# Optimization experiments

Hardware: AMD Instinct MI355X
Metric: run time of the kernel (lower is better)

The kernel has to match this reference:

```python
import jax, jax.numpy as jnp
import numpy as np

B, L, K, I, O = 4, 10000, 16, 256, 256


def setup_inputs() -> dict:
    key = jax.random.key(0)
    k1, k2, k3 = jax.random.split(key, 3)
    x = jax.random.normal(k1, (B, L, I), dtype=jnp.float32)
    index_tensor = jax.random.randint(k2, (L, K), 0, L, dtype=jnp.int64)
    stdv = 0.5
    mask = jax.random.uniform(k3, (K, I, O), dtype=jnp.float32, minval=-stdv, maxval=stdv)
    bias = jnp.zeros((O,), dtype=jnp.float32)
    return {"x": x, "index_tensor": index_tensor, "mask": mask, "bias": bias}


def reference(x, index_tensor, mask, bias):
    # torch: expand x to [b,l,l,i], gather along dim2 with index[l,k] -> [b,l,k,i]
    # equivalent: per output node n, neighbors x[:, index_tensor[n, j], :]
    gathered = x[:, index_tensor, :]            # [b, l, k, i]
    # flatten(k,i) @ flatten(mask: [k*i, o]) == einsum over k,i
    y = jnp.einsum('blki,kio->blo', gathered, mask) + bias
    return y
```

## Files before the change

### kernel.cpp

```cpp
#include <hip/hip_runtime.h>

#define Bdim 4
#define Ldim 10000
#define Kdim 16
#define Idim 256
#define Odim 256

typedef __attribute__((ext_vector_type(8))) __bf16 bf16x8;
typedef __attribute__((ext_vector_type(4))) float f32x4;

__global__ __launch_bounds__(256)
void prepack(const float* __restrict__ x, const float* __restrict__ mask,
             __bf16* __restrict__ xb, __bf16* __restrict__ wpk)
{
    const int b = blockIdx.x;
    if (b < 2500) {
        const size_t base = ((size_t)b * 256 + threadIdx.x) * 16;
#pragma unroll
        for (int j = 0; j < 2; ++j) {
            const float4 f0 = *(const float4*)(x + base + j * 8);
            const float4 f1 = *(const float4*)(x + base + j * 8 + 4);
            bf16x8 v;
            v[0] = (__bf16)f0.x; v[1] = (__bf16)f0.y; v[2] = (__bf16)f0.z; v[3] = (__bf16)f0.w;
            v[4] = (__bf16)f1.x; v[5] = (__bf16)f1.y; v[6] = (__bf16)f1.z; v[7] = (__bf16)f1.w;
            *(bf16x8*)(xb + base + j * 8) = v;
        }
    } else {
        const int tg = (b - 2500) * 256 + threadIdx.x;
        const int c  = tg >> 6;
        const int ln = tg & 63;
        const int ni  = c & 3;
        const int ks  = (c >> 2) & 1;
        const int wid = (c >> 3) & 3;
        const int kb  = c >> 5;
        const int n   = wid * 64 + ni * 16 + (ln & 15);
        const int kk0 = kb * 64 + ks * 32 + (ln >> 4) * 8;
        bf16x8 v;
#pragma unroll
        for (int j = 0; j < 8; ++j)
            v[j] = (__bf16)mask[(size_t)(kk0 + j) * Odim + n];
        *(bf16x8*)(wpk + (size_t)tg * 8) = v;
    }
}

#define TL 8
#define BM 32
#define LDA 72

#define BARRIER() do { asm volatile("s_waitcnt lgkmcnt(0)" ::: "memory"); \
                       __builtin_amdgcn_s_barrier(); } while (0)

__global__ __launch_bounds__(256, 4)
void piconv_gemm(const __bf16* __restrict__ xb,
                 const int* __restrict__ idxT,
                 const __bf16* __restrict__ wpk,
                 const float* __restrict__ bias,
                 float* __restrict__ out)
{
    __shared__ __bf16 Alds[2][BM * LDA];
    __shared__ int    idx_lds[TL * Kdim];

    const int t    = threadIdx.x;
    const int l0   = blockIdx.x * TL;
    const int lane = t & 63;
    const int wid  = t >> 6;
    const int q    = lane >> 4;
    const int r16  = lane & 15;

    if (t < TL * Kdim)
        idx_lds[t] = idxT[l0 * Kdim + t];

    const int arow = t >> 3;
    const int apart = t & 7;
    const int alt  = arow & 7;
    const int abb  = arow >> 3;
    const size_t abase = ((size_t)abb * Ldim) << 8;

    const __bf16* wbase = wpk + ((size_t)(wid * 8) << 9) + lane * 8;

    f32x4  acc[2][4] = {};
    bf16x8 a0, a1;
    bf16x8 wA[8], wB[8];

    __syncthreads();

    {
        const int iv = idx_lds[alt * Kdim];
        const __bf16* s0 = xb + abase + (((size_t)iv) << 8) + apart * 8;
        a0 = *(const bf16x8*)s0;
#pragma unroll
        for (int j = 0; j < 8; ++j)
            wA[j] = *(const bf16x8*)(wbase + j * 512);
        a1 = *(const bf16x8*)(s0 + 64);
    }

#define STEP(S, BUF, AV, WCUR, WNXT, PFA, PFW)                                  \
    {                                                                           \
        *(bf16x8*)&Alds[BUF][arow * LDA + apart * 8] = AV;                      \
        BARRIER();                                                              \
        if (PFA) {                        \
            const int kn = ((S) + 2) >> 2;                                      \
            const int io = ((((S) + 2) & 3) << 6) + apart * 8;                  \
            const int iv = idx_lds[alt * Kdim + kn];                            \
            AV = *(const bf16x8*)(xb + abase + (((size_t)iv) << 8) + io);       \
        }                                                                       \
        if (PFW) {                                                  \
            const __bf16* wq = wbase + ((size_t)((S) + 1)) * 16384;             \
            _Pragma("unroll")                                                   \
            for (int j = 0; j < 8; ++j)                                         \
                WNXT[j] = *(const bf16x8*)(wq + j * 512);                       \
        }                                                                       \
        _Pragma("unroll")                                                       \
        for (int ks = 0; ks < 2; ++ks) {                                        \
            bf16x8 af[2];                                                       \
            _Pragma("unroll")                                                   \
            for (int mi = 0; mi < 2; ++mi)                                      \
                af[mi] = *(bf16x8*)&Alds[BUF][(mi * 16 + r16) * LDA + ks * 32 + q * 8]; \
            _Pragma("unroll")                                                   \
            for (int mi = 0; mi < 2; ++mi)                                      \
                _Pragma("unroll")                                               \
                for (int ni = 0; ni < 4; ++ni)                                  \
                    acc[mi][ni] = __builtin_amdgcn_mfma_f32_16x16x32_bf16(      \
                        af[mi], WCUR[ks * 4 + ni], acc[mi][ni], 0, 0, 0);       \
        }                                                                       \
    }

    for (int s2 = 0; s2 < 31; ++s2) {
        STEP(2 * s2,     0, a0, wA, wB, true, true)
        STEP(2 * s2 + 1, 1, a1, wB, wA, true, true)
    }
    STEP(62, 0, a0, wA, wB, false, true)
    STEP(63, 1, a1, wB, wA, false, false)
#undef STEP

    float bv[4];
#pragma unroll
    for (int ni = 0; ni < 4; ++ni)
        bv[ni] = bias[wid * 64 + ni * 16 + r16];
#pragma unroll
    for (int mi = 0; mi < 2; ++mi) {
#pragma unroll
        for (int rr = 0; rr < 4; ++rr) {
            const int g  = mi * 16 + q * 4 + rr;
            const int bb = g >> 3;
            const int lt = g & 7;
            float* dst = out + (((size_t)(bb * Ldim + l0 + lt)) << 8) + wid * 64 + r16;
#pragma unroll
            for (int ni = 0; ni < 4; ++ni)
                dst[ni * 16] = acc[mi][ni][rr] + bv[ni];
        }
    }
}

#define FTL 32
#define FBN 128
#define FLDA 72
__global__ __launch_bounds__(256)
void piconv_fallback(const float* __restrict__ x,
                     const int* __restrict__ idxT,
                     const float* __restrict__ mask,
                     const float* __restrict__ bias,
                     float* __restrict__ out)
{
    __shared__ __bf16 Alds[128 * FLDA];
    __shared__ __bf16 Wlds[FBN * FLDA];
    const int t  = threadIdx.x;
    const int l0 = blockIdx.x * FTL;
    const int n0 = blockIdx.y * FBN;
    const int lane = t & 63;
    const int wid  = t >> 6;
    const int wm   = wid >> 1;
    const int wn   = wid & 1;
    const int q    = lane >> 4;
    const int r16  = lane & 15;
    f32x4 acc[4][4] = {};
    const int am    = t >> 1;
    const int ahalf = t & 1;
    const int alt   = am & 31;
    const int abb   = am >> 5;
    const int al    = l0 + alt;
    const bool avalid = (al < Ldim);
    for (int kb = 0; kb < 64; ++kb) {
        {
            const int ksl = kb >> 2;
            const int i0  = ((kb & 3) << 6) + (ahalf << 5);
            const int idx = avalid ? idxT[al * Kdim + ksl] : 0;
            const float* src = x + (((size_t)(abb * Ldim + idx)) << 8) + i0;
#pragma unroll
            for (int j = 0; j < 4; ++j) {
                const float4 f0 = *(const float4*)(src + j * 8);
                const float4 f1 = *(const float4*)(src + j * 8 + 4);
                bf16x8 v;
                v[0] = (__bf16)f0.x; v[1] = (__bf16)f0.y; v[2] = (__bf16)f0.z; v[3] = (__bf16)f0.w;
                v[4] = (__bf16)f1.x; v[5] = (__bf16)f1.y; v[6] = (__bf16)f1.z; v[7] = (__bf16)f1.w;
                *(bf16x8*)&Alds[am * FLDA + (ahalf << 5) + j * 8] = v;
            }
        }
        {
#pragma unroll
            for (int it = 0; it < 4; ++it) {
                const int pair = t + it * 256;
                const int n    = pair & 127;
                const int g    = pair >> 7;
                const float* src = mask + (((size_t)(kb * 64 + g * 8)) << 8) + n0 + n;
                bf16x8 v;
#pragma unroll
                for (int j = 0; j < 8; ++j)
                    v[j] = (__bf16)src[(size_t)j << 8];
                *(bf16x8*)&Wlds[n * FLDA + g * 8] = v;
            }
        }
        __syncthreads();
#pragma unroll
        for (int ks = 0; ks < 2; ++ks) {
            bf16x8 af[4], bfr[4];
#pragma unroll
            for (int mi = 0; mi < 4; ++mi)
                af[mi] = *(bf16x8*)&Alds[(wm * 64 + mi * 16 + r16) * FLDA + ks * 32 + q * 8];
#pragma unroll
            for (int ni = 0; ni < 4; ++ni)
                bfr[ni] = *(bf16x8*)&Wlds[(wn * 64 + ni * 16 + r16) * FLDA + ks * 32 + q * 8];
#pragma unroll
            for (int mi = 0; mi < 4; ++mi)
#pragma unroll
                for (int ni = 0; ni < 4; ++ni)
                    acc[mi][ni] = __builtin_amdgcn_mfma_f32_16x16x32_bf16(
                        af[mi], bfr[ni], acc[mi][ni], 0, 0, 0);
        }
        __syncthreads();
    }
    float bv[4];
#pragma unroll
    for (int ni = 0; ni < 4; ++ni)
        bv[ni] = bias[n0 + wn * 64 + ni * 16 + r16];
#pragma unroll
    for (int mi = 0; mi < 4; ++mi) {
        const int mrow = wm * 64 + mi * 16 + q * 4;
#pragma unroll
        for (int rr = 0; rr < 4; ++rr) {
            const int m  = mrow + rr;
            const int lt = m & 31;
            const int bb = m >> 5;
            const int l  = l0 + lt;
            if (l < Ldim) {
                float* dst = out + (((size_t)(bb * Ldim + l)) << 8) + n0 + wn * 64 + r16;
#pragma unroll
                for (int ni = 0; ni < 4; ++ni)
                    dst[ni * 16] = acc[mi][ni][rr] + bv[ni];
            }
        }
    }
}

extern "C" void kernel_launch(void* const* d_in, const int* in_sizes, int n_in,
                              void* d_out, int out_size, void* d_ws, size_t ws_size,
                              hipStream_t stream) {
    const float* x    = (const float*)d_in[0];
    const int*   idx  = (const int*)d_in[1];
    const float* mask = (const float*)d_in[2];
    const float* bias = (const float*)d_in[3];
    float* out = (float*)d_out;

    const size_t xb_bytes = (size_t)Bdim * Ldim * Idim * 2;
    const size_t wp_bytes = (size_t)Kdim * Idim * Odim * 2;

    if (ws_size >= xb_bytes + wp_bytes) {
        __bf16* xb  = (__bf16*)d_ws;
        __bf16* wpk = (__bf16*)((char*)d_ws + xb_bytes);
        prepack<<<2500 + 512, 256, 0, stream>>>(x, mask, xb, wpk);
        piconv_gemm<<<Ldim / TL, 256, 0, stream>>>(xb, idx, wpk, bias, out);
    } else {
        dim3 grid((Ldim + FTL - 1) / FTL, Odim / FBN, 1);
        piconv_fallback<<<grid, 256, 0, stream>>>(x, idx, mask, bias, out);
    }
}
```

Measured before the change: 211.2 us.

## Enlarge gather-GEMM M tile to 80 rows with fragment-ordered LDS layout

Each block now handles 20 output positions (80 rows across batches) instead of 8 (32 rows). Every weight fragment loaded from global memory is reused across five MFMA row tiles rather than two, reducing weight traffic per output. The A tile in LDS is stored in MFMA-fragment order with no padding, and the index table uses a padded stride, to avoid bank conflicts. The gather prefetch is now one step ahead instead of two. In exchange, register pressure rises (launch bounds drop to 2 blocks per SIMD), occupancy falls, and the A loads leave some threads idle.

```diff
diff --git a/kernel.cpp b/kernel.cpp
--- a/kernel.cpp
+++ b/kernel.cpp
@@ -43,22 +43,22 @@
     }
 }
 
-#define TL 8
-#define BM 32
-#define LDA 72
+#define TL 20
+#define BM 80
+#define IDXS 17
 
 #define BARRIER() do { asm volatile("s_waitcnt lgkmcnt(0)" ::: "memory"); \
                        __builtin_amdgcn_s_barrier(); } while (0)
 
-__global__ __launch_bounds__(256, 4)
+__global__ __launch_bounds__(256, 2)
 void piconv_gemm(const __bf16* __restrict__ xb,
                  const int* __restrict__ idxT,
                  const __bf16* __restrict__ wpk,
                  const float* __restrict__ bias,
                  float* __restrict__ out)
 {
-    __shared__ __bf16 Alds[2][BM * LDA];
-    __shared__ int    idx_lds[TL * Kdim];
+    __shared__ __bf16 Alds[2][BM * 64];
+    __shared__ int    idx_lds[TL * IDXS];
 
     const int t    = threadIdx.x;
     const int l0   = blockIdx.x * TL;
@@ -67,42 +67,71 @@
     const int q    = lane >> 4;
     const int r16  = lane & 15;
 
-    if (t < TL * Kdim)
-        idx_lds[t] = idxT[l0 * Kdim + t];
-
-    const int arow = t >> 3;
-    const int apart = t & 7;
-    const int alt  = arow & 7;
-    const int abb  = arow >> 3;
-    const size_t abase = ((size_t)abb * Ldim) << 8;
+    {
+        const int e0 = t;
+        idx_lds[(e0 >> 4) * IDXS + (e0 & 15)] = idxT[l0 * Kdim + e0];
+        if (t < 64) {
+            const int e1 = t + 256;
+            idx_lds[(e1 >> 4) * IDXS + (e1 & 15)] = idxT[l0 * Kdim + e1];
+        }
+    }
+
+    const int rA = t & 31,               pA = t >> 5;
+    const int rB = 32 + (t & 31);
+    const int rC = 64 + ((t >> 1) & 15);
+    const bool cAct = (t & 1) == 0;
+    const int abbA = rA / TL, altA = rA % TL;
+    const int abbB = rB / TL, altB = rB % TL;
+    const int abbC = rC / TL, altC = rC % TL;
+    const size_t abaseA = ((size_t)abbA * Ldim) << 8;
+    const size_t abaseB = ((size_t)abbB * Ldim) << 8;
+    const size_t abaseC = ((size_t)abbC * Ldim) << 8;
+    const int dsA = (((rA >> 4) * 2 + (pA >> 2)) * 512) + ((pA & 3) * 128) + ((rA & 15) * 8);
+    const int dsB = (((rB >> 4) * 2 + (pA >> 2)) * 512) + ((pA & 3) * 128) + ((rB & 15) * 8);
+    const int dsC = (((rC >> 4) * 2 + (pA >> 2)) * 512) + ((pA & 3) * 128) + ((rC & 15) * 8);
+    const int po  = pA * 8;
 
     const __bf16* wbase = wpk + ((size_t)(wid * 8) << 9) + lane * 8;
 
-    f32x4  acc[2][4] = {};
-    bf16x8 a0, a1;
+    f32x4  acc[5][4] = {};
+    bf16x8 aRA, aRB, aRC;
     bf16x8 wA[8], wB[8];
 
     __syncthreads();
 
     {
-        const int iv = idx_lds[alt * Kdim];
-        const __bf16* s0 = xb + abase + (((size_t)iv) << 8) + apart * 8;
-        a0 = *(const bf16x8*)s0;
+        const int ivA = idx_lds[altA * IDXS];
+        const int ivB = idx_lds[altB * IDXS];
+        aRA = *(const bf16x8*)(xb + abaseA + (((size_t)ivA) << 8) + po);
+        aRB = *(const bf16x8*)(xb + abaseB + (((size_t)ivB) << 8) + po);
+        if (cAct) {
+            const int ivC = idx_lds[altC * IDXS];
+            aRC = *(const bf16x8*)(xb + abaseC + (((size_t)ivC) << 8) + po);
+        }
 #pragma unroll
         for (int j = 0; j < 8; ++j)
             wA[j] = *(const bf16x8*)(wbase + j * 512);
-        a1 = *(const bf16x8*)(s0 + 64);
-    }
-
-#define STEP(S, BUF, AV, WCUR, WNXT, PFA, PFW)                                  \
+    }
+
+#define STEP(S, WCUR, WNXT, PFA, PFW)                                           \
     {                                                                           \
-        *(bf16x8*)&Alds[BUF][arow * LDA + apart * 8] = AV;                      \
+        __bf16* db = &Alds[(S) & 1][0];                                         \
+        *(bf16x8*)(db + dsA) = aRA;                                             \
+        *(bf16x8*)(db + dsB) = aRB;                                             \
+        if (cAct) *(bf16x8*)(db + dsC) = aRC;                                   \
         BARRIER();                                                              \
-        if (PFA) {                        \
-            const int kn = ((S) + 2) >> 2;                                      \
-            const int io = ((((S) + 2) & 3) << 6) + apart * 8;                  \
-            const int iv = idx_lds[alt * Kdim + kn];                            \
-            AV = *(const bf16x8*)(xb + abase + (((size_t)iv) << 8) + io);       \
+        if (PFA) {                                           \
+            const int T   = (S) + 1;                                            \
+            const int kn  = T >> 2;                                             \
+            const int iob = ((T & 3) << 6) + po;                                \
+            const int ivA = idx_lds[altA * IDXS + kn];                          \
+            const int ivB = idx_lds[altB * IDXS + kn];                          \
+            aRA = *(const bf16x8*)(xb + abaseA + (((size_t)ivA) << 8) + iob);   \
+            aRB = *(const bf16x8*)(xb + abaseB + (((size_t)ivB) << 8) + iob);   \
+            if (cAct) {                                                         \
+                const int ivC = idx_lds[altC * IDXS + kn];                      \
+                aRC = *(const bf16x8*)(xb + abaseC + (((size_t)ivC) << 8) + iob); \
+            }                                                                   \
         }                                                                       \
         if (PFW) {                                                  \
             const __bf16* wq = wbase + ((size_t)((S) + 1)) * 16384;             \
@@ -112,12 +141,12 @@
         }                                                                       \
         _Pragma("unroll")                                                       \
         for (int ks = 0; ks < 2; ++ks) {                                        \
-            bf16x8 af[2];                                                       \
+            bf16x8 af[5];                                                       \
             _Pragma("unroll")                                                   \
-            for (int mi = 0; mi < 2; ++mi)                                      \
-                af[mi] = *(bf16x8*)&Alds[BUF][(mi * 16 + r16) * LDA + ks * 32 + q * 8]; \
+            for (int mi = 0; mi < 5; ++mi)                                      \
+                af[mi] = *(const bf16x8*)(&Alds[(S) & 1][(mi * 2 + ks) * 512 + lane * 8]); \
             _Pragma("unroll")                                                   \
-            for (int mi = 0; mi < 2; ++mi)                                      \
+            for (int mi = 0; mi < 5; ++mi)                                      \
                 _Pragma("unroll")                                               \
                 for (int ni = 0; ni < 4; ++ni)                                  \
                     acc[mi][ni] = __builtin_amdgcn_mfma_f32_16x16x32_bf16(      \
@@ -126,11 +155,11 @@
     }
 
     for (int s2 = 0; s2 < 31; ++s2) {
-        STEP(2 * s2,     0, a0, wA, wB, true, true)
-        STEP(2 * s2 + 1, 1, a1, wB, wA, true, true)
-    }
-    STEP(62, 0, a0, wA, wB, false, true)
-    STEP(63, 1, a1, wB, wA, false, false)
+        STEP(2 * s2,     wA, wB, true, true)
+        STEP(2 * s2 + 1, wB, wA, true, true)
+    }
+    STEP(62, wA, wB, true,  true)
+    STEP(63, wB, wA, false, false)
 #undef STEP
 
     float bv[4];
@@ -138,13 +167,13 @@
     for (int ni = 0; ni < 4; ++ni)
         bv[ni] = bias[wid * 64 + ni * 16 + r16];
 #pragma unroll
-    for (int mi = 0; mi < 2; ++mi) {
+    for (int mi = 0; mi < 5; ++mi) {
 #pragma unroll
         for (int rr = 0; rr < 4; ++rr) {
-            const int g  = mi * 16 + q * 4 + rr;
-            const int bb = g >> 3;
-            const int lt = g & 7;
-            float* dst = out + (((size_t)(bb * Ldim + l0 + lt)) << 8) + wid * 64 + r16;
+            const int r  = mi * 16 + q * 4 + rr;
+            const int ab = r / TL;
+            const int al = r % TL;
+            float* dst = out + (((size_t)(ab * Ldim + l0 + al)) << 8) + wid * 64 + r16;
 #pragma unroll
             for (int ni = 0; ni < 4; ++ni)
                 dst[ni * 16] = acc[mi][ni][rr] + bv[ni];
```

Result: faster. 178.8 us (-15.3%).
